# Kernel tuning notes

Measured on AMD Instinct MI355X. Metric: run time of the kernel, lower is better.

Reference implementation:

```python
import jax, jax.numpy as jnp
import numpy as np

B, C, H, W = 8, 128, 128, 128
P = 32768
STRIDE = (1.0, 1.0)
TOKEN_FORMAT = 'xy'


def setup_inputs() -> dict:
    key = jax.random.key(0)
    k1, k2 = jax.random.split(key)
    # points mostly in-range [0, W-1], with some out-of-bounds to exercise masking
    tk_codes = jax.random.uniform(k1, (B, P, 2), dtype=jnp.float32, minval=-2.0, maxval=130.0)
    feat_grid = jax.random.normal(k2, (B, C, H, W), dtype=jnp.float32)
    return {"tk_codes": tk_codes, "feat_grid": feat_grid}


def reference(tk_codes, feat_grid):
    b, c, h, w = feat_grid.shape
    pts = tk_codes[..., :2].astype(jnp.float32)
    pts = pts / jnp.array([STRIDE[0], STRIDE[1]], dtype=jnp.float32)
    lead_shape = pts.shape[:-1]
    pts = pts.reshape(b, -1, 2)  # [B, P, 2]
    x, y = pts[..., 0], pts[..., 1]

    # zero weight for out-of-bounds points (matches sequential mask assignments)
    in_bounds = (x >= 0) & (y >= 0) & (x <= w - 1) & (y <= h - 1)  # [B, P]

    fx, cx = jnp.floor(x), jnp.ceil(x)
    fy, cy = jnp.floor(y), jnp.ceil(y)
    # 4 corners in order (floor,floor), (floor,ceil), (ceil,floor), (ceil,ceil) on (x, y)
    corner_x = jnp.stack([fx, fx, cx, cx], axis=2)  # [B, P, 4]
    corner_y = jnp.stack([fy, cy, fy, cy], axis=2)

    gx = jnp.fmod(corner_x.astype(jnp.int32), w)
    gy = jnp.fmod(corner_y.astype(jnp.int32), h)
    gx = jnp.maximum(gx, 0)
    gy = jnp.maximum(gy, 0)

    # inverse-distance weights to the (wrapped/clamped) integer corners
    dx = pts[:, :, None, 0] - gx.astype(jnp.float32)
    dy = pts[:, :, None, 1] - gy.astype(jnp.float32)
    dist_inv = 1.0 / (jnp.sqrt(dx * dx + dy * dy) + 1e-10)  # [B, P, 4]
    wgt = in_bounds[..., None].astype(jnp.float32) * dist_inv
    denom = jnp.sum(wgt, axis=-1, keepdims=True)
    denom = jnp.where(denom == 0.0, 1.0, denom)
    wgt = wgt / denom

    if TOKEN_FORMAT == 'xy':
        flat_idx = gy * w + gx  # [B, P, 4]
    else:  # 'hw'
        flat_idx = gx * w + gy

    fg = jnp.transpose(feat_grid, (0, 2, 3, 1)).reshape(b, h * w, c)  # [B, HW, C]
    vals = jnp.take_along_axis(fg, flat_idx.reshape(b, -1, 1), axis=1)  # [B, P*4, C]
    vals = vals.reshape(b, -1, 4, c)
    out = jnp.sum(vals * wgt[..., None], axis=2)  # [B, P, C]
    return out.reshape(*lead_shape, c)
```

## Files before the change

### kernel.cpp

```cpp
#include <hip/hip_runtime.h>

#define BB 8
#define CC 128
#define HH 128
#define WW 128
#define PP 32768
#define HWW (HH * WW)

typedef float v4f __attribute__((ext_vector_type(4)));

__device__ inline unsigned short cvt_bf16_rne(float f) {
    unsigned int u = __float_as_uint(f);
    unsigned int r = (u + 0x7fffu + ((u >> 16) & 1u)) >> 16;
    return (unsigned short)r;
}

__global__ __launch_bounds__(256) void transpose_bf16_kernel(
    const float* __restrict__ in,
    unsigned short* __restrict__ out)
{
    __shared__ float tile[32][132];
    const int b = blockIdx.y;
    const int sBase = blockIdx.x * 32;
    const int tid = threadIdx.x;

    const float* inb = in + (size_t)b * CC * HWW;
    unsigned short* outb = out + (size_t)b * HWW * CC;

    const int tx = tid & 7;
    const int c0 = tid >> 3;
#pragma unroll
    for (int i = 0; i < 4; ++i) {
        const int c = c0 + 32 * i;
        const v4f v = *(const v4f*)(inb + (size_t)c * HWW + sBase + 4 * tx);
#pragma unroll
        for (int j = 0; j < 4; ++j)
            tile[4 * tx + j][c] = v[j];
    }
    __syncthreads();

    const int cx = tid & 31;
    const int s0 = tid >> 5;
#pragma unroll
    for (int i = 0; i < 4; ++i) {
        const int s = s0 + 8 * i;
        const v4f v = *(const v4f*)&tile[s][4 * cx];
        ushort4 h;
        h.x = cvt_bf16_rne(v[0]);
        h.y = cvt_bf16_rne(v[1]);
        h.z = cvt_bf16_rne(v[2]);
        h.w = cvt_bf16_rne(v[3]);
        *(ushort4*)(outb + (size_t)(sBase + s) * CC + 4 * cx) = h;
    }
}

__device__ inline void compute_corners(float x, float y,
                                       int gx[4], int gy[4], float wgt[4])
{
    const bool inb = (x >= 0.f) && (y >= 0.f) &&
                     (x <= (float)(WW - 1)) && (y <= (float)(HH - 1));
    const float fx = floorf(x), cx = ceilf(x);
    const float fy = floorf(y), cy = ceilf(y);
    const float corx[4] = {fx, fx, cx, cx};
    const float cory[4] = {fy, cy, fy, cy};
    float denom = 0.f;
#pragma unroll
    for (int k = 0; k < 4; ++k) {
        int gxi = ((int)corx[k]) % WW;
        int gyi = ((int)cory[k]) % HH;
        if (gxi < 0) gxi = 0;
        if (gyi < 0) gyi = 0;
        const float dx = x - (float)gxi;
        const float dy = y - (float)gyi;
        const float dinv = __builtin_amdgcn_rcpf(sqrtf(dx * dx + dy * dy) + 1e-10f);
        const float w = inb ? dinv : 0.f;
        gx[k] = gxi;
        gy[k] = gyi;
        wgt[k] = w;
        denom += w;
    }
    const float rden = (denom == 0.f) ? 1.f : __builtin_amdgcn_rcpf(denom);
#pragma unroll
    for (int k = 0; k < 4; ++k) wgt[k] *= rden;
}

__global__ __launch_bounds__(256) void weights_kernel(
    const float* __restrict__ tk,
    int4* __restrict__ idx_out,
    float4* __restrict__ wgt_out)
{
    const int p = blockIdx.x * 256 + (int)threadIdx.x;
    const float2 xy = ((const float2*)tk)[p];

    int gx[4], gy[4];
    float wgt[4];
    compute_corners(xy.x, xy.y, gx, gy, wgt);

    int4 id;
    id.x = gy[0] * WW + gx[0];
    id.y = gy[1] * WW + gx[1];
    id.z = gy[2] * WW + gx[2];
    id.w = gy[3] * WW + gx[3];
    idx_out[p] = id;
    wgt_out[p] = make_float4(wgt[0], wgt[1], wgt[2], wgt[3]);
}

__global__ __launch_bounds__(256) void gather_bf16_kernel(
    const unsigned short* __restrict__ grid,
    const int4* __restrict__ idxs,
    const float4* __restrict__ wgts,
    float* __restrict__ out)
{
    const int blk = blockIdx.x;
    const int b = blk & 7;
    const int inner = blk >> 3;
    const int wave = (int)threadIdx.x >> 6;
    const int half = ((int)threadIdx.x >> 5) & 1;
    const int sub = (int)threadIdx.x & 31;

    const int p = b * PP + inner * 8 + wave * 2 + half;

    const int4 id = idxs[p];
    const float4 w = wgts[p];

    const unsigned short* gb = grid + (size_t)b * HWW * CC;
    const int idk[4] = {id.x, id.y, id.z, id.w};
    const float wk[4] = {w.x, w.y, w.z, w.w};

    v4f acc = {0.f, 0.f, 0.f, 0.f};
#pragma unroll
    for (int k = 0; k < 4; ++k) {
        const uint2 u = *(const uint2*)(gb + (size_t)idk[k] * CC + 4 * sub);
        v4f v;
        v[0] = __uint_as_float(u.x << 16);
        v[1] = __uint_as_float(u.x & 0xffff0000u);
        v[2] = __uint_as_float(u.y << 16);
        v[3] = __uint_as_float(u.y & 0xffff0000u);
        acc += wk[k] * v;
    }
    __builtin_nontemporal_store(acc, (v4f*)out + (size_t)p * (CC / 4) + sub);
}

__global__ __launch_bounds__(256) void gather_nchw_kernel(
    const float* __restrict__ tk,
    const float* __restrict__ grid,
    float* __restrict__ out)
{
    const int wave = (int)((blockIdx.x * blockDim.x + threadIdx.x) >> 6);
    const int lane = threadIdx.x & 63;
    if (wave >= BB * PP) return;
    const int b = wave >> 15;

    const float2 xy = ((const float2*)tk)[wave];
    int gx[4], gy[4];
    float wgt[4];
    compute_corners(xy.x, xy.y, gx, gy, wgt);

    const float* gb = grid + (size_t)b * CC * HWW;
    const int c0 = lane * 2;
    float a0 = 0.f, a1 = 0.f;
#pragma unroll
    for (int k = 0; k < 4; ++k) {
        const int sidx = gy[k] * WW + gx[k];
        a0 += wgt[k] * gb[(size_t)c0 * HWW + sidx];
        a1 += wgt[k] * gb[(size_t)(c0 + 1) * HWW + sidx];
    }
    ((float2*)out)[(size_t)wave * (CC / 2) + lane] = make_float2(a0, a1);
}

extern "C" void kernel_launch(void* const* d_in, const int* in_sizes, int n_in,
                              void* d_out, int out_size, void* d_ws, size_t ws_size,
                              hipStream_t stream) {
    const float* tk = (const float*)d_in[0];
    const float* fg = (const float*)d_in[1];
    float* out = (float*)d_out;

    const size_t gridBytes = (size_t)BB * HWW * CC * 2;
    const size_t idxBytes  = (size_t)BB * PP * sizeof(int4);
    const size_t wgtBytes  = (size_t)BB * PP * sizeof(float4);
    const size_t need = gridBytes + idxBytes + wgtBytes;

    if (ws_size >= need) {
        unsigned short* gbf = (unsigned short*)d_ws;
        int4*   idxs = (int4*)((char*)d_ws + gridBytes);
        float4* wgts = (float4*)((char*)d_ws + gridBytes + idxBytes);

        dim3 tg(HWW / 32, BB);
        transpose_bf16_kernel<<<tg, 256, 0, stream>>>(fg, gbf);
        weights_kernel<<<(BB * PP) / 256, 256, 0, stream>>>(tk, idxs, wgts);
        gather_bf16_kernel<<<(BB * PP) / 8, 256, 0, stream>>>(gbf, idxs, wgts, out);
    } else {
        const int blocks = (BB * PP * 64) / 256;
        gather_nchw_kernel<<<blocks, 256, 0, stream>>>(tk, fg, out);
    }
}
```

Measured before the change: 202.7 us.

## Fuse weight computation into gather and widen transpose tiles with swizzled LDS

The separate weights kernel is removed. Each 16-lane group now computes its point's corners and weights inline and loads 16-byte bf16 chunks per lane, which eliminates the index/weight workspace round-trip and one launch. The transpose now handles 64 spatial positions per block with an XOR-swizzled shared tile to cut bank conflicts, uses nontemporal input loads, and writes 16-byte packed bf16 outputs. The cost is that corner math is recomputed redundantly by the 16 lanes of each point, and the LDS footprint per block doubles.

After: 207.8 us. 1.03x slower.

```diff
diff --git a/kernel.cpp b/kernel.cpp
--- a/kernel.cpp
+++ b/kernel.cpp
@@ -19,38 +19,46 @@
     const float* __restrict__ in,
     unsigned short* __restrict__ out)
 {
-    __shared__ float tile[32][132];
-    const int b = blockIdx.y;
-    const int sBase = blockIdx.x * 32;
+    __shared__ float tile[64][132];
+    const int blk = blockIdx.x;
+    const int b = blk & 7;
+    const int chunk = blk >> 3;
+    const int sBase = chunk * 64;
     const int tid = threadIdx.x;
 
     const float* inb = in + (size_t)b * CC * HWW;
     unsigned short* outb = out + (size_t)b * HWW * CC;
 
-    const int tx = tid & 7;
-    const int c0 = tid >> 3;
+    const int tx = tid & 15;
+    const int c0 = tid >> 4;
+    const int xw = (tx & 3) << 3;
 #pragma unroll
-    for (int i = 0; i < 4; ++i) {
-        const int c = c0 + 32 * i;
-        const v4f v = *(const v4f*)(inb + (size_t)c * HWW + sBase + 4 * tx);
+    for (int i = 0; i < 8; ++i) {
+        const int c = c0 + 16 * i;
+        const v4f v = __builtin_nontemporal_load(
+            (const v4f*)(inb + (size_t)c * HWW + sBase + 4 * tx));
+        const int xc = c ^ xw;
 #pragma unroll
         for (int j = 0; j < 4; ++j)
-            tile[4 * tx + j][c] = v[j];
+            tile[4 * tx + j][xc] = v[j];
     }
     __syncthreads();
 
-    const int cx = tid & 31;
-    const int s0 = tid >> 5;
+    const int cx = tid & 15;
+    const int s0 = tid >> 4;
 #pragma unroll
     for (int i = 0; i < 4; ++i) {
-        const int s = s0 + 8 * i;
-        const v4f v = *(const v4f*)&tile[s][4 * cx];
-        ushort4 h;
-        h.x = cvt_bf16_rne(v[0]);
-        h.y = cvt_bf16_rne(v[1]);
-        h.z = cvt_bf16_rne(v[2]);
-        h.w = cvt_bf16_rne(v[3]);
-        *(ushort4*)(outb + (size_t)(sBase + s) * CC + 4 * cx) = h;
+        const int s = s0 + 16 * i;
+        const int xv = ((s >> 2) & 3) << 3;
+        const int base = (8 * cx) ^ xv;
+        const v4f a = *(const v4f*)&tile[s][base];
+        const v4f d = *(const v4f*)&tile[s][base + 4];
+        uint4 h;
+        h.x = (unsigned)cvt_bf16_rne(a[0]) | ((unsigned)cvt_bf16_rne(a[1]) << 16);
+        h.y = (unsigned)cvt_bf16_rne(a[2]) | ((unsigned)cvt_bf16_rne(a[3]) << 16);
+        h.z = (unsigned)cvt_bf16_rne(d[0]) | ((unsigned)cvt_bf16_rne(d[1]) << 16);
+        h.w = (unsigned)cvt_bf16_rne(d[2]) | ((unsigned)cvt_bf16_rne(d[3]) << 16);
+        *(uint4*)(outb + (size_t)(sBase + s) * CC + 8 * cx) = h;
     }
 }
 
@@ -84,61 +92,46 @@
     for (int k = 0; k < 4; ++k) wgt[k] *= rden;
 }
 
-__global__ __launch_bounds__(256) void weights_kernel(
+__global__ __launch_bounds__(256) void gather_fused_kernel(
     const float* __restrict__ tk,
-    int4* __restrict__ idx_out,
-    float4* __restrict__ wgt_out)
-{
-    const int p = blockIdx.x * 256 + (int)threadIdx.x;
-    const float2 xy = ((const float2*)tk)[p];
-
-    int gx[4], gy[4];
-    float wgt[4];
-    compute_corners(xy.x, xy.y, gx, gy, wgt);
-
-    int4 id;
-    id.x = gy[0] * WW + gx[0];
-    id.y = gy[1] * WW + gx[1];
-    id.z = gy[2] * WW + gx[2];
-    id.w = gy[3] * WW + gx[3];
-    idx_out[p] = id;
-    wgt_out[p] = make_float4(wgt[0], wgt[1], wgt[2], wgt[3]);
-}
-
-__global__ __launch_bounds__(256) void gather_bf16_kernel(
     const unsigned short* __restrict__ grid,
-    const int4* __restrict__ idxs,
-    const float4* __restrict__ wgts,
     float* __restrict__ out)
 {
     const int blk = blockIdx.x;
     const int b = blk & 7;
     const int inner = blk >> 3;
-    const int wave = (int)threadIdx.x >> 6;
-    const int half = ((int)threadIdx.x >> 5) & 1;
-    const int sub = (int)threadIdx.x & 31;
+    const int grp = (int)threadIdx.x >> 4;
+    const int l = (int)threadIdx.x & 15;
 
-    const int p = b * PP + inner * 8 + wave * 2 + half;
+    const int p = b * PP + inner * 16 + grp;
+    const float2 xy = ((const float2*)tk)[p];
 
-    const int4 id = idxs[p];
-    const float4 w = wgts[p];
+    int gx[4], gy[4];
+    float w[4];
+    compute_corners(xy.x, xy.y, gx, gy, w);
 
     const unsigned short* gb = grid + (size_t)b * HWW * CC;
-    const int idk[4] = {id.x, id.y, id.z, id.w};
-    const float wk[4] = {w.x, w.y, w.z, w.w};
-
-    v4f acc = {0.f, 0.f, 0.f, 0.f};
+    v4f acc0 = {0.f, 0.f, 0.f, 0.f};
+    v4f acc1 = {0.f, 0.f, 0.f, 0.f};
 #pragma unroll
     for (int k = 0; k < 4; ++k) {
-        const uint2 u = *(const uint2*)(gb + (size_t)idk[k] * CC + 4 * sub);
-        v4f v;
-        v[0] = __uint_as_float(u.x << 16);
-        v[1] = __uint_as_float(u.x & 0xffff0000u);
-        v[2] = __uint_as_float(u.y << 16);
-        v[3] = __uint_as_float(u.y & 0xffff0000u);
-        acc += wk[k] * v;
+        const int id = gy[k] * WW + gx[k];
+        const uint4 u = *(const uint4*)(gb + (size_t)id * CC + 8 * l);
+        v4f v0, v1;
+        v0[0] = __uint_as_float(u.x << 16);
+        v0[1] = __uint_as_float(u.x & 0xffff0000u);
+        v0[2] = __uint_as_float(u.y << 16);
+        v0[3] = __uint_as_float(u.y & 0xffff0000u);
+        v1[0] = __uint_as_float(u.z << 16);
+        v1[1] = __uint_as_float(u.z & 0xffff0000u);
+        v1[2] = __uint_as_float(u.w << 16);
+        v1[3] = __uint_as_float(u.w & 0xffff0000u);
+        acc0 += w[k] * v0;
+        acc1 += w[k] * v1;
     }
-    __builtin_nontemporal_store(acc, (v4f*)out + (size_t)p * (CC / 4) + sub);
+    v4f* ob = (v4f*)(out + (size_t)p * CC + 8 * l);
+    __builtin_nontemporal_store(acc0, ob);
+    __builtin_nontemporal_store(acc1, ob + 1);
 }
 
 __global__ __launch_bounds__(256) void gather_nchw_kernel(
@@ -176,19 +169,12 @@
     float* out = (float*)d_out;
 
     const size_t gridBytes = (size_t)BB * HWW * CC * 2;
-    const size_t idxBytes  = (size_t)BB * PP * sizeof(int4);
-    const size_t wgtBytes  = (size_t)BB * PP * sizeof(float4);
-    const size_t need = gridBytes + idxBytes + wgtBytes;
 
-    if (ws_size >= need) {
+    if (ws_size >= gridBytes) {
         unsigned short* gbf = (unsigned short*)d_ws;
-        int4*   idxs = (int4*)((char*)d_ws + gridBytes);
-        float4* wgts = (float4*)((char*)d_ws + gridBytes + idxBytes);
 
-        dim3 tg(HWW / 32, BB);
-        transpose_bf16_kernel<<<tg, 256, 0, stream>>>(fg, gbf);
-        weights_kernel<<<(BB * PP) / 256, 256, 0, stream>>>(tk, idxs, wgts);
-        gather_bf16_kernel<<<(BB * PP) / 8, 256, 0, stream>>>(gbf, idxs, wgts, out);
+        transpose_bf16_kernel<<<(BB * HWW) / 64, 256, 0, stream>>>(fg, gbf);
+        gather_fused_kernel<<<(BB * PP) / 16, 256, 0, stream>>>(tk, gbf, out);
     } else {
         const int blocks = (BB * PP * 64) / 256;
         gather_nchw_kernel<<<blocks, 256, 0, stream>>>(tk, fg, out);
```
